# Kernel tuning notes

Measured on AMD Instinct MI355X. Metric: run time of the kernel, lower is better.

The kernel has to match this reference:

```python
import jax, jax.numpy as jnp
import numpy as np

B, S, D = 1, 2048, 4096
H, HKV, HD = 32, 8, 128
MAX_SEQ = 4096
EPS = 1e-5


def rmsnorm(x, w, eps=EPS):
    var = jnp.mean(x * x, axis=-1, keepdims=True)
    return w * (x * jax.lax.rsqrt(var + eps))


def rotate_half_interleaved(x):
    x1 = x[..., ::2]
    x2 = x[..., 1::2]
    return jnp.stack((-x2, x1), axis=-1).reshape(x.shape)


def setup_inputs() -> dict:
    key = jax.random.key(0)
    ks = jax.random.split(key, 8)
    hidden_states = jax.random.normal(ks[0], (B, S, D), dtype=jnp.float32)
    # realistic interleaved RoPE tables: each frequency repeated twice along head_dim
    inv_freq = 1.0 / (10000.0 ** (np.arange(0, HD, 2, dtype=np.float32) / HD))
    pos = np.arange(S, dtype=np.float32)
    ang = pos[:, None] * inv_freq[None, :]            # [S, HD/2]
    ang = np.repeat(ang, 2, axis=-1)                   # [S, HD] interleaved
    cos = jnp.asarray(np.cos(ang))[None].repeat(B, axis=0)  # [B, S, HD]
    sin = jnp.asarray(np.sin(ang))[None].repeat(B, axis=0)
    scale = 1.0 / np.sqrt(D)
    return {
        "hidden_states": hidden_states,
        "cos": cos,
        "sin": sin,
        "k_cache": jnp.zeros((B, MAX_SEQ, HKV, HD), dtype=jnp.float32),
        "v_cache": jnp.zeros((B, MAX_SEQ, HKV, HD), dtype=jnp.float32),
        "Wq": jax.random.normal(ks[1], (D, H * HD), dtype=jnp.float32) * scale,
        "Wk": jax.random.normal(ks[2], (D, HKV * HD), dtype=jnp.float32) * scale,
        "Wv": jax.random.normal(ks[3], (D, HKV * HD), dtype=jnp.float32) * scale,
        "Wo": jax.random.normal(ks[4], (H * HD, D), dtype=jnp.float32) * scale,
        "rms_weight": jnp.ones((D,), dtype=jnp.float32),
        "position_ids": jnp.arange(S, dtype=jnp.int64 if jax.config.jax_enable_x64 else jnp.int32),
        "seq_len": S,
    }


def reference(hidden_states, cos, sin, k_cache, v_cache, Wq, Wk, Wv, Wo,
              rms_weight, position_ids, seq_len):
    residual = hidden_states
    h = rmsnorm(hidden_states, rms_weight)
    b, s = h.shape[:2]

    q = jnp.einsum('bsd,de->bse', h, Wq).reshape(b, s, H, HD)
    k = jnp.einsum('bsd,de->bse', h, Wk).reshape(b, s, HKV, HD)
    v = jnp.einsum('bsd,de->bse', h, Wv).reshape(b, s, HKV, HD)

    # interleaved RoPE, cos/sin broadcast over head axis (unsqueeze_dim=-2)
    c = cos[:, :, None, :]
    si = sin[:, :, None, :]
    q = q * c + rotate_half_interleaved(q) * si
    k = k * c + rotate_half_interleaved(k) * si

    # KV-cache scatter at position_ids (repeat_factor == 1 here)
    k_cache_new = k_cache.at[:, position_ids].set(k)
    v_cache_new = v_cache.at[:, position_ids].set(v)

    # prefill path (new_tok_seq_len > 1): causal SDPA with GQA over fresh K/V
    group = H // HKV
    k_full = jnp.repeat(k, group, axis=2)  # [b, s, H, HD]
    v_full = jnp.repeat(v, group, axis=2)
    qh = q.transpose(0, 2, 1, 3)           # bhqd
    kh = k_full.transpose(0, 2, 1, 3)
    vh = v_full.transpose(0, 2, 1, 3)
    scores = jnp.einsum('bhqd,bhkd->bhqk', qh, kh) / jnp.sqrt(jnp.float32(HD))
    causal = jnp.tril(jnp.ones((s, s), dtype=bool))
    scores = jnp.where(causal[None, None], scores, jnp.finfo(scores.dtype).min)
    probs = jax.nn.softmax(scores, axis=-1)
    attn = jnp.einsum('bhqk,bhkd->bhqd', probs, vh)
    attn = attn.transpose(0, 2, 1, 3).reshape(b, s, H * HD)

    out = jnp.einsum('bse,ed->bsd', attn, Wo)
    with_residual = residual + out
    return with_residual, k_cache_new, v_cache_new
```

## Files before the change

### kernel.cpp

```cpp
#include <hip/hip_runtime.h>
#include <hip/hip_bf16.h>
#include <cstdint>

#define S_LEN 2048
#define DMODEL 4096
#define NHEAD 32
#define NKV 8
#define HDIM 128
#define MAXSEQ 4096
#define NQKV 6144

typedef __bf16 bf16x8 __attribute__((ext_vector_type(8)));
typedef float f32x4 __attribute__((ext_vector_type(4)));
typedef short s16x4 __attribute__((ext_vector_type(4)));

__device__ __forceinline__ short f2bf(float f) {
  unsigned u = __builtin_bit_cast(unsigned, f);
  u += 0x7fffu + ((u >> 16) & 1u);
  return (short)(u >> 16);
}

__device__ __forceinline__ void gload_lds16(const void* g, const void* l) {
  __builtin_amdgcn_global_load_lds((const __attribute__((address_space(1))) unsigned*)g,
                                   (__attribute__((address_space(3))) unsigned*)(l), 16, 0, 0);
}

__global__ __launch_bounds__(256) void rmsnorm_kernel(const float* __restrict__ x,
                                                      const float* __restrict__ w,
                                                      short* __restrict__ out) {
  const int row = blockIdx.x, tid = threadIdx.x;
  const float4* xr = (const float4*)(x + (size_t)row * DMODEL);
  const float4* wr = (const float4*)w;
  float4 v[4];
  float ss = 0.f;
#pragma unroll
  for (int i = 0; i < 4; ++i) {
    v[i] = xr[tid + i * 256];
    ss += v[i].x * v[i].x + v[i].y * v[i].y + v[i].z * v[i].z + v[i].w * v[i].w;
  }
#pragma unroll
  for (int m = 32; m; m >>= 1) ss += __shfl_down(ss, m, 64);
  __shared__ float red[4];
  if ((tid & 63) == 0) red[tid >> 6] = ss;
  __syncthreads();
  float tot = red[0] + red[1] + red[2] + red[3];
  float sc = rsqrtf(tot * (1.f / DMODEL) + 1e-5f);
#pragma unroll
  for (int i = 0; i < 4; ++i) {
    float4 wv = wr[tid + i * 256];
    s16x4 o;
    o[0] = f2bf(v[i].x * sc * wv.x);
    o[1] = f2bf(v[i].y * sc * wv.y);
    o[2] = f2bf(v[i].z * sc * wv.z);
    o[3] = f2bf(v[i].w * sc * wv.w);
    *(s16x4*)&out[(size_t)row * DMODEL + (size_t)(tid + i * 256) * 4] = o;
  }
}

__global__ __launch_bounds__(256) void cast_transpose(const float* __restrict__ src,
                                                      short* __restrict__ dst,
                                                      int rows, int cols) {
  __shared__ float tile[32][33];
  const int c0 = blockIdx.x * 32, r0 = blockIdx.y * 32;
  const int tx = threadIdx.x, ty = threadIdx.y;
#pragma unroll
  for (int i = ty; i < 32; i += 8) tile[i][tx] = src[(size_t)(r0 + i) * cols + c0 + tx];
  __syncthreads();
  const int tid = ty * 32 + tx;
#pragma unroll
  for (int rep = 0; rep < 2; ++rep) {
    int w = rep * 256 + tid;
    int i = w >> 4, pr = (w & 15) * 2;
    short2 o;
    o.x = f2bf(tile[pr][i]);
    o.y = f2bf(tile[pr + 1][i]);
    *(short2*)&dst[(size_t)(c0 + i) * rows + r0 + pr] = o;
  }
}

__global__ __launch_bounds__(256) void v_transpose(const float* __restrict__ QKV,
                                                   float* __restrict__ vc,
                                                   short* __restrict__ vt) {
  __shared__ float tile[32][33];
  const int d0 = blockIdx.x * 32, s0 = blockIdx.y * 32, g = blockIdx.z;
  const int tx = threadIdx.x, ty = threadIdx.y;
#pragma unroll
  for (int i = ty; i < 32; i += 8) {
    float v = QKV[(size_t)(s0 + i) * NQKV + (NHEAD + NKV) * HDIM + g * HDIM + d0 + tx];
    tile[i][tx] = v;
    vc[(size_t)(s0 + i) * (NKV * HDIM) + g * HDIM + d0 + tx] = v;
  }
  __syncthreads();
  const int tid = ty * 32 + tx;
#pragma unroll
  for (int rep = 0; rep < 2; ++rep) {
    int w = rep * 256 + tid;
    int i = w >> 4, pr = (w & 15) * 2;
    short2 o;
    o.x = f2bf(tile[pr][i]);
    o.y = f2bf(tile[pr + 1][i]);
    *(short2*)&vt[((size_t)g * HDIM + d0 + i) * S_LEN + s0 + pr] = o;
  }
}


template<int KS, int MH>
__device__ __forceinline__ void ph_load(const short* __restrict__ AsH, const short* __restrict__ BsH,
                                        const int lrow, const int quad, const int brow0,
                                        bf16x8 (&aR)[4], bf16x8 (&bR)[2][4]) {
  const int xr = lrow & 7;
#pragma unroll
  for (int f = 0; f < 4; ++f)
    aR[f] = *(const bf16x8*)&AsH[((((MH * 4 + f) * 16 + lrow) * 8) + ((KS * 4 + quad) ^ xr)) * 8];
  if constexpr (KS == 0 && MH == 0) {
#pragma unroll
    for (int ks = 0; ks < 2; ++ks)
#pragma unroll
      for (int f = 0; f < 4; ++f)
        bR[ks][f] = *(const bf16x8*)&BsH[(((brow0 + f * 16 + lrow) * 8) + ((ks * 4 + quad) ^ xr)) * 8];
  }
}

template<int KS, int MH>
__device__ __forceinline__ void ph_mfma(bf16x8 (&aR)[4], bf16x8 (&bR)[2][4], f32x4 (&acc)[8][4]) {
#pragma unroll
  for (int f = 0; f < 4; ++f)
#pragma unroll
    for (int n = 0; n < 4; ++n)
      acc[MH * 4 + f][n] =
          __builtin_amdgcn_mfma_f32_16x16x32_bf16(aR[f], bR[KS][n], acc[MH * 4 + f][n], 0, 0, 0);
}

__global__ __launch_bounds__(512, 2) void gemm256(const short* __restrict__ A,
                                                  const short* __restrict__ Bt,
                                                  float* __restrict__ C,
                                                  const float* __restrict__ resid,
                                                  int M, int N, int K) {
  extern __shared__ __align__(16) short smem[];
  short* As = smem;
  short* Bs = smem + 32768;
  const int tid = threadIdx.x;
  const int lane = tid & 63, wave = tid >> 6;
  const int wm = wave >> 2, wn = wave & 3;
  const int lrow = lane & 15, quad = lane >> 4;
  const int bhalf = wn >> 1, brow0 = (wn & 1) * 64;
  const int m0 = blockIdx.y * 256, n0 = blockIdx.x * 256;
  const int srow = tid >> 3;
  const int scol = ((tid & 7) ^ (srow & 7)) << 3;
  const short* Ag = A + (size_t)m0 * K;
  const short* Bg = Bt + (size_t)n0 * K;
  const int nk = K >> 6;

#define STAGE_A(b, h, kt) do { \
    const short* g_ = Ag + (size_t)((h) * 128 + srow) * K + (size_t)(kt) * 64 + scol; \
    short* l_ = As + ((b) * 2 + (h)) * 8192 + wave * 512; \
    gload_lds16(g_, l_); \
    gload_lds16(g_ + (size_t)64 * K, l_ + 4096); \
  } while (0)
#define STAGE_B(b, h, kt) do { \
    const short* g_ = Bg + (size_t)((h) * 128 + srow) * K + (size_t)(kt) * 64 + scol; \
    short* l_ = Bs + ((b) * 2 + (h)) * 8192 + wave * 512; \
    gload_lds16(g_, l_); \
    gload_lds16(g_ + (size_t)64 * K, l_ + 4096); \
  } while (0)
#define VW_NONE
#define VW_4 asm volatile("s_waitcnt vmcnt(4)" ::: "memory");
#define VW_COND if (more) { asm volatile("s_waitcnt vmcnt(4)" ::: "memory"); } \
                else      { asm volatile("s_waitcnt vmcnt(0)" ::: "memory"); }
#define PHASE(BUF, KS, MH, STMT, VW) \
  ph_load<KS, MH>(As + ((BUF) * 2 + wm) * 8192, Bs + ((BUF) * 2 + bhalf) * 8192, \
                  lrow, quad, brow0, aR, bR); \
  STMT; \
  VW \
  __builtin_amdgcn_s_barrier(); \
  asm volatile("s_waitcnt lgkmcnt(0)" ::: "memory"); \
  __builtin_amdgcn_s_setprio(1); \
  ph_mfma<KS, MH>(aR, bR, acc); \
  __builtin_amdgcn_s_setprio(0); \
  __builtin_amdgcn_s_barrier();

  f32x4 acc[8][4] = {};
  bf16x8 aR[4], bR[2][4];

  STAGE_A(0, 0, 0); STAGE_A(0, 1, 0);
  STAGE_B(0, 0, 0); STAGE_B(0, 1, 0);
  STAGE_B(1, 0, 1); STAGE_B(1, 1, 1);
  asm volatile("s_waitcnt vmcnt(4)" ::: "memory");
  __builtin_amdgcn_s_barrier();

  const int niter = nk >> 1;
  for (int i = 0; i < niter; ++i) {
    const int t = 2 * i;
    const bool more = (t + 2 < nk);
    PHASE(0, 0, 0, STAGE_A(1, 0, t + 1), VW_NONE)
    PHASE(0, 0, 1, STAGE_A(1, 1, t + 1), VW_NONE)
    PHASE(0, 1, 0, if (more) { STAGE_B(0, 0, t + 2); }, VW_NONE)
    PHASE(0, 1, 1, if (more) { STAGE_B(0, 1, t + 2); }, VW_COND)
    PHASE(1, 0, 0, if (more) { STAGE_A(0, 0, t + 2); }, VW_NONE)
    PHASE(1, 0, 1, if (more) { STAGE_A(0, 1, t + 2); }, VW_NONE)
    PHASE(1, 1, 0, if (more) { STAGE_B(1, 0, t + 3); }, VW_NONE)
    PHASE(1, 1, 1, if (more) { STAGE_B(1, 1, t + 3); }, VW_4)
  }

#pragma unroll
  for (int fm = 0; fm < 8; ++fm)
#pragma unroll
    for (int fn = 0; fn < 4; ++fn) {
      int row = m0 + wm * 128 + fm * 16 + quad * 4;
      int col = n0 + wn * 64 + fn * 16 + lrow;
#pragma unroll
      for (int r = 0; r < 4; ++r) {
        float v = acc[fm][fn][r];
        size_t o = (size_t)(row + r) * N + col;
        if (resid) v += resid[o];
        C[o] = v;
      }
    }
#undef STAGE_A
#undef STAGE_B
#undef VW_NONE
#undef VW_4
#undef VW_COND
#undef PHASE
}

__global__ __launch_bounds__(256) void rope_kernel(const float* __restrict__ QKV,
                                                   const float* __restrict__ cosb,
                                                   const float* __restrict__ sinb,
                                                   short* __restrict__ qo,
                                                   short* __restrict__ ko,
                                                   float* __restrict__ kc,
                                                   float* __restrict__ vc) {
  const int s = blockIdx.x, tid = threadIdx.x;
  const float4* r4 = (const float4*)(QKV + (size_t)s * NQKV);
  const float qscale = 0.08838834764831845f;
#pragma unroll
  for (int it = 0; it < 5; ++it) {
    int i = it * 256 + tid;
    float4 x = r4[i];
    int e = i * 4;
    int d = e & 127;
    float4 c = *(const float4*)&cosb[(size_t)s * HDIM + d];
    float4 si = *(const float4*)&sinb[(size_t)s * HDIM + d];
    float o0 = x.x * c.x - x.y * si.x;
    float o1 = x.y * c.y + x.x * si.y;
    float o2 = x.z * c.z - x.w * si.z;
    float o3 = x.w * c.w + x.z * si.w;
    if (e < NHEAD * HDIM) {
      int hh = e >> 7;
      s16x4 ov;
      ov[0] = f2bf(o0 * qscale); ov[1] = f2bf(o1 * qscale);
      ov[2] = f2bf(o2 * qscale); ov[3] = f2bf(o3 * qscale);
      *(s16x4*)&qo[((size_t)hh * S_LEN + s) * HDIM + d] = ov;
    } else {
      int ek = e - NHEAD * HDIM;
      int g = ek >> 7;
      s16x4 ov;
      ov[0] = f2bf(o0); ov[1] = f2bf(o1); ov[2] = f2bf(o2); ov[3] = f2bf(o3);
      *(s16x4*)&ko[((size_t)g * S_LEN + s) * HDIM + d] = ov;
      *(float4*)&kc[(size_t)s * (NKV * HDIM) + ek] = make_float4(o0, o1, o2, o3);
    }
  }
  {
    const size_t base = (size_t)S_LEN * NKV * HDIM;
    const size_t i = (size_t)s * 256 + tid;
    const float4 z = make_float4(0.f, 0.f, 0.f, 0.f);
    ((float4*)(kc + base))[i] = z;
    ((float4*)(vc + base))[i] = z;
  }
}

#define TKEY 128
__global__ __launch_bounds__(256, 1) void attn_kernel(const short* __restrict__ Q,
                                                      const short* __restrict__ Kb,
                                                      const short* __restrict__ Vt,
                                                      short* __restrict__ out) {
  extern __shared__ __align__(16) short smem[];
  short* Ks = smem;
  short* Vs = smem + 32768;
  short* Ps = smem + 65536;
  const int tid = threadIdx.x;
  const int lane = tid & 63, wave = tid >> 6;
  const int lrow = lane & 15, quad = lane >> 4;
  const int g = blockIdx.x & 7, p = blockIdx.x >> 3;
  const int h = g * 4 + wave;
  const float L2E = 1.44269504f;
  const short* Kg = Kb + (size_t)g * S_LEN * HDIM;
  const short* Vg = Vt + (size_t)g * HDIM * S_LEN;
  short* Pw = Ps + wave * 1024;

#pragma unroll 1
  for (int ph = 0; ph < 2; ++ph) {
    const int qt = ph ? (63 - p) : p;
    const int nt = (qt >> 2) + 1;

    bf16x8 qf[2][4];
#pragma unroll
    for (int i = 0; i < 2; ++i)
#pragma unroll
      for (int kf = 0; kf < 4; ++kf)
        qf[i][kf] = *(const bf16x8*)&Q[((size_t)h * S_LEN + qt * 32 + i * 16 + lrow) * HDIM + kf * 32 + quad * 8];

    f32x4 O[2][8] = {};
    float mrun[2][4], lrun[2][4];
#pragma unroll
    for (int i = 0; i < 2; ++i)
#pragma unroll
      for (int r = 0; r < 4; ++r) { mrun[i][r] = -1e30f; lrun[i][r] = 0.f; }

#pragma unroll
    for (int ii = 0; ii < 8; ++ii) {
      int s = (wave * 8 + ii) * 64 + lane;
      int r = s >> 4, gg = (s & 15) ^ (r & 15);
      gload_lds16(Kg + (size_t)r * HDIM + gg * 8, Ks + (wave * 8 + ii) * 512);
    }
#pragma unroll
    for (int ii = 0; ii < 8; ++ii) {
      int s = (wave * 8 + ii) * 64 + lane;
      int d = s >> 4, kg = (s & 15) ^ (d & 15);
      gload_lds16(Vg + (size_t)d * S_LEN + kg * 8, Vs + (wave * 8 + ii) * 512);
    }
    __syncthreads();

#pragma unroll 1
    for (int t = 0; t < nt; ++t) {
      const int bsel = t & 1;
      if (t + 1 < nt) {
        const int kb2 = (t + 1) * TKEY, o = (1 - bsel) * 16384;
#pragma unroll
        for (int ii = 0; ii < 8; ++ii) {
          int s = (wave * 8 + ii) * 64 + lane;
          int r = s >> 4, gg = (s & 15) ^ (r & 15);
          gload_lds16(Kg + (size_t)(kb2 + r) * HDIM + gg * 8, Ks + o + (wave * 8 + ii) * 512);
        }
#pragma unroll
        for (int ii = 0; ii < 8; ++ii) {
          int s = (wave * 8 + ii) * 64 + lane;
          int d = s >> 4, kg = (s & 15) ^ (d & 15);
          gload_lds16(Vg + (size_t)d * S_LEN + kb2 + kg * 8, Vs + o + (wave * 8 + ii) * 512);
        }
      }
      const short* Kc = Ks + bsel * 16384;
      const short* Vc = Vs + bsel * 16384;

      f32x4 sc[2][8] = {};
#pragma unroll
      for (int c = 0; c < 8; ++c) {
        int r = c * 16 + lrow;
#pragma unroll
        for (int kf = 0; kf < 4; ++kf) {
          int slot = r * 16 + ((kf * 4 + quad) ^ lrow);
          bf16x8 kfr = *(const bf16x8*)&Kc[slot * 8];
          sc[0][c] = __builtin_amdgcn_mfma_f32_16x16x32_bf16(qf[0][kf], kfr, sc[0][c], 0, 0, 0);
          sc[1][c] = __builtin_amdgcn_mfma_f32_16x16x32_bf16(qf[1][kf], kfr, sc[1][c], 0, 0, 0);
        }
      }

      const int kb = t * TKEY;
      const bool last = (t == nt - 1);
#pragma unroll
      for (int i = 0; i < 2; ++i) {
        if (last) {
#pragma unroll
          for (int c = 0; c < 8; ++c) {
            int key = kb + c * 16 + lrow;
#pragma unroll
            for (int r = 0; r < 4; ++r) {
              int row = qt * 32 + i * 16 + quad * 4 + r;
              if (key > row) sc[i][c][r] = -1e30f;
            }
          }
        }
        float tm[4];
#pragma unroll
        for (int r = 0; r < 4; ++r) tm[r] = sc[i][0][r];
#pragma unroll
        for (int c = 1; c < 8; ++c)
#pragma unroll
          for (int r = 0; r < 4; ++r) tm[r] = fmaxf(tm[r], sc[i][c][r]);
#pragma unroll
        for (int msk = 1; msk <= 8; msk <<= 1)
#pragma unroll
          for (int r = 0; r < 4; ++r) tm[r] = fmaxf(tm[r], __shfl_xor(tm[r], msk, 64));
#pragma unroll
        for (int r = 0; r < 4; ++r) {
          float nm = fmaxf(mrun[i][r], tm[r]);
          float alpha = exp2f((mrun[i][r] - nm) * L2E);
          mrun[i][r] = nm;
          lrun[i][r] *= alpha;
#pragma unroll
          for (int jd = 0; jd < 8; ++jd) O[i][jd][r] *= alpha;
        }
        float rs[4] = {0.f, 0.f, 0.f, 0.f};
#pragma unroll
        for (int c = 0; c < 8; ++c)
#pragma unroll
          for (int r = 0; r < 4; ++r) {
            float pv = exp2f((sc[i][c][r] - mrun[i][r]) * L2E);
            sc[i][c][r] = pv;
            rs[r] += pv;
          }
#pragma unroll
        for (int msk = 1; msk <= 8; msk <<= 1)
#pragma unroll
          for (int r = 0; r < 4; ++r) rs[r] += __shfl_xor(rs[r], msk, 64);
#pragma unroll
        for (int r = 0; r < 4; ++r) lrun[i][r] += rs[r];
      }

#pragma unroll
      for (int ks = 0; ks < 4; ++ks) {
#pragma unroll
        for (int i = 0; i < 2; ++i)
#pragma unroll
          for (int cc = 0; cc < 2; ++cc) {
            int c = ks * 2 + cc;
            int kg = cc * 2 + (lrow >> 3), off = lrow & 7;
#pragma unroll
            for (int r = 0; r < 4; ++r) {
              int q2 = i * 16 + quad * 4 + r;
              int slot = q2 * 4 + (kg ^ (q2 & 3) ^ ((q2 >> 2) & 3));
              Pw[slot * 8 + off] = f2bf(sc[i][c][r]);
            }
          }
        bf16x8 pa[2];
#pragma unroll
        for (int i = 0; i < 2; ++i) {
          int q2 = i * 16 + lrow;
          int slot = q2 * 4 + (quad ^ (q2 & 3) ^ ((q2 >> 2) & 3));
          pa[i] = *(const bf16x8*)&Pw[slot * 8];
        }
#pragma unroll
        for (int jd = 0; jd < 8; ++jd) {
          int d = jd * 16 + lrow;
          int slotv = d * 16 + ((ks * 4 + quad) ^ lrow);
          bf16x8 vb = *(const bf16x8*)&Vc[slotv * 8];
          O[0][jd] = __builtin_amdgcn_mfma_f32_16x16x32_bf16(pa[0], vb, O[0][jd], 0, 0, 0);
          O[1][jd] = __builtin_amdgcn_mfma_f32_16x16x32_bf16(pa[1], vb, O[1][jd], 0, 0, 0);
        }
      }
      __syncthreads();
    }

#pragma unroll
    for (int i = 0; i < 2; ++i)
#pragma unroll
      for (int r = 0; r < 4; ++r) {
        float inv = 1.f / lrun[i][r];
        int row = qt * 32 + i * 16 + quad * 4 + r;
#pragma unroll
        for (int jd = 0; jd < 8; ++jd)
          out[(size_t)row * DMODEL + h * HDIM + jd * 16 + lrow] = f2bf(O[i][jd][r] * inv);
      }
    __syncthreads();
  }
}

extern "C" void kernel_launch(void* const* d_in, const int* in_sizes, int n_in,
                              void* d_out, int out_size, void* d_ws, size_t ws_size,
                              hipStream_t stream) {
  const float* hs   = (const float*)d_in[0];
  const float* cosb = (const float*)d_in[1];
  const float* sinb = (const float*)d_in[2];
  const float* Wq   = (const float*)d_in[5];
  const float* Wk   = (const float*)d_in[6];
  const float* Wv   = (const float*)d_in[7];
  const float* Wo   = (const float*)d_in[8];
  const float* rmsw = (const float*)d_in[9];

  float* outp = (float*)d_out;
  float* kc = outp + (size_t)S_LEN * DMODEL;
  float* vc = kc + (size_t)MAXSEQ * NKV * HDIM;

  char* p = (char*)d_ws;
  short* h_bf  = (short*)p; p += (size_t)S_LEN * DMODEL * 2;
  short* WqkvT = (short*)p; p += (size_t)NQKV * DMODEL * 2;
  short* WoT   = (short*)p; p += (size_t)DMODEL * DMODEL * 2;
  float* QKV   = (float*)p; p += (size_t)S_LEN * NQKV * 4;
  short* q_bf  = (short*)p; p += (size_t)NHEAD * S_LEN * HDIM * 2;
  short* k_bf  = (short*)p; p += (size_t)NKV * S_LEN * HDIM * 2;
  short* vt_bf = (short*)p; p += (size_t)NKV * HDIM * S_LEN * 2;
  short* attn_bf = h_bf;

  const int ATTN_LDS = 139264;
  hipFuncSetAttribute(reinterpret_cast<const void*>(attn_kernel),
                      hipFuncAttributeMaxDynamicSharedMemorySize, ATTN_LDS);
  const int GEMM_LDS = 131072;
  hipFuncSetAttribute(reinterpret_cast<const void*>(gemm256),
                      hipFuncAttributeMaxDynamicSharedMemorySize, GEMM_LDS);

  rmsnorm_kernel<<<S_LEN, 256, 0, stream>>>(hs, rmsw, h_bf);
  cast_transpose<<<dim3(DMODEL / 32, DMODEL / 32), dim3(32, 8), 0, stream>>>(Wq, WqkvT, DMODEL, DMODEL);
  cast_transpose<<<dim3(1024 / 32, DMODEL / 32), dim3(32, 8), 0, stream>>>(Wk, WqkvT + (size_t)DMODEL * DMODEL, DMODEL, 1024);
  cast_transpose<<<dim3(1024 / 32, DMODEL / 32), dim3(32, 8), 0, stream>>>(Wv, WqkvT + (size_t)5120 * DMODEL, DMODEL, 1024);
  cast_transpose<<<dim3(DMODEL / 32, DMODEL / 32), dim3(32, 8), 0, stream>>>(Wo, WoT, DMODEL, DMODEL);
  gemm256<<<dim3(NQKV / 256, S_LEN / 256), 512, GEMM_LDS, stream>>>(h_bf, WqkvT, QKV, nullptr, S_LEN, NQKV, DMODEL);
  rope_kernel<<<S_LEN, 256, 0, stream>>>(QKV, cosb, sinb, q_bf, k_bf, kc, vc);
  v_transpose<<<dim3(HDIM / 32, S_LEN / 32, NKV), dim3(32, 8), 0, stream>>>(QKV, vc, vt_bf);
  attn_kernel<<<256, 256, ATTN_LDS, stream>>>(q_bf, k_bf, vt_bf, attn_bf);
  gemm256<<<dim3(DMODEL / 256, S_LEN / 256), 512, GEMM_LDS, stream>>>(attn_bf, WoT, outp, hs, S_LEN, DMODEL, DMODEL);
}
```

Before: 675.3 us.

## Templatize GEMM N-tile width and merge weight cast-transpose launches

The 256x256 GEMM gets a template parameter for N fragments per wave, so the QKV projection uses 256x192 tiles (256 blocks) and the output projection uses 256x128 tiles (256 blocks). The aim is to fill all CUs, where 256-wide N tiles left too few blocks (192 and 128). B-tile staging, the LDS layout and the vmcnt waits are reworked for a variable number of 64-row B groups. The four weight cast-transpose launches become one 3D-grid launch with early exit for out-of-range blocks. Narrower N tiles lower arithmetic intensity per block and add A-tile reloads.

```diff
diff --git a/kernel.cpp b/kernel.cpp
--- a/kernel.cpp
+++ b/kernel.cpp
@@ -23,6 +23,14 @@
 __device__ __forceinline__ void gload_lds16(const void* g, const void* l) {
   __builtin_amdgcn_global_load_lds((const __attribute__((address_space(1))) unsigned*)g,
                                    (__attribute__((address_space(3))) unsigned*)(l), 16, 0, 0);
+}
+
+template<int N> __device__ __forceinline__ void vwait() {
+  if constexpr (N == 0) asm volatile("s_waitcnt vmcnt(0)" ::: "memory");
+  else if constexpr (N == 1) asm volatile("s_waitcnt vmcnt(1)" ::: "memory");
+  else if constexpr (N == 2) asm volatile("s_waitcnt vmcnt(2)" ::: "memory");
+  else if constexpr (N == 3) asm volatile("s_waitcnt vmcnt(3)" ::: "memory");
+  else if constexpr (N == 4) asm volatile("s_waitcnt vmcnt(4)" ::: "memory");
 }
 
 __global__ __launch_bounds__(256) void rmsnorm_kernel(const float* __restrict__ x,
@@ -57,11 +65,23 @@
   }
 }
 
-__global__ __launch_bounds__(256) void cast_transpose(const float* __restrict__ src,
-                                                      short* __restrict__ dst,
-                                                      int rows, int cols) {
+__global__ __launch_bounds__(256) void cast_transpose_all(const float* __restrict__ Wq,
+                                                          const float* __restrict__ Wk,
+                                                          const float* __restrict__ Wv,
+                                                          const float* __restrict__ Wo,
+                                                          short* __restrict__ WqkvT,
+                                                          short* __restrict__ WoT) {
+  const int z = blockIdx.z;
+  const float* src;
+  short* dst;
+  int cols;
+  if (z == 0)      { src = Wq; dst = WqkvT;                            cols = 4096; }
+  else if (z == 1) { src = Wk; dst = WqkvT + (size_t)4096 * 4096;      cols = 1024; }
+  else if (z == 2) { src = Wv; dst = WqkvT + (size_t)5120 * 4096;      cols = 1024; }
+  else             { src = Wo; dst = WoT;                              cols = 4096; }
+  const int c0 = blockIdx.x * 32, r0 = blockIdx.y * 32;
+  if (c0 >= cols) return;
   __shared__ float tile[32][33];
-  const int c0 = blockIdx.x * 32, r0 = blockIdx.y * 32;
   const int tx = threadIdx.x, ty = threadIdx.y;
 #pragma unroll
   for (int i = ty; i < 32; i += 8) tile[i][tx] = src[(size_t)(r0 + i) * cols + c0 + tx];
@@ -74,7 +94,7 @@
     short2 o;
     o.x = f2bf(tile[pr][i]);
     o.y = f2bf(tile[pr + 1][i]);
-    *(short2*)&dst[(size_t)(c0 + i) * rows + r0 + pr] = o;
+    *(short2*)&dst[(size_t)(c0 + i) * 4096 + r0 + pr] = o;
   }
 }
 
@@ -104,33 +124,34 @@
 }
 
 
-template<int KS, int MH>
-__device__ __forceinline__ void ph_load(const short* __restrict__ AsH, const short* __restrict__ BsH,
-                                        const int lrow, const int quad, const int brow0,
-                                        bf16x8 (&aR)[4], bf16x8 (&bR)[2][4]) {
+template<int NF, int KS, int MH>
+__device__ __forceinline__ void ph_load(const short* __restrict__ AsH, const short* __restrict__ BsB,
+                                        const int lrow, const int quad, const int wn,
+                                        bf16x8 (&aR)[4], bf16x8 (&bR)[2][NF]) {
   const int xr = lrow & 7;
 #pragma unroll
   for (int f = 0; f < 4; ++f)
     aR[f] = *(const bf16x8*)&AsH[((((MH * 4 + f) * 16 + lrow) * 8) + ((KS * 4 + quad) ^ xr)) * 8];
-  if constexpr (KS == 0 && MH == 0) {
-#pragma unroll
-    for (int ks = 0; ks < 2; ++ks)
-#pragma unroll
-      for (int f = 0; f < 4; ++f)
-        bR[ks][f] = *(const bf16x8*)&BsH[(((brow0 + f * 16 + lrow) * 8) + ((ks * 4 + quad) ^ xr)) * 8];
-  }
-}
-
-template<int KS, int MH>
-__device__ __forceinline__ void ph_mfma(bf16x8 (&aR)[4], bf16x8 (&bR)[2][4], f32x4 (&acc)[8][4]) {
+  if constexpr (MH == 0) {
+#pragma unroll
+    for (int f = 0; f < NF; ++f) {
+      int rB = wn * (16 * NF) + f * 16 + lrow;
+      bR[KS][f] = *(const bf16x8*)&BsB[((rB * 8) + ((KS * 4 + quad) ^ xr)) * 8];
+    }
+  }
+}
+
+template<int NF, int KS, int MH>
+__device__ __forceinline__ void ph_mfma(bf16x8 (&aR)[4], bf16x8 (&bR)[2][NF], f32x4 (&acc)[8][NF]) {
 #pragma unroll
   for (int f = 0; f < 4; ++f)
 #pragma unroll
-    for (int n = 0; n < 4; ++n)
+    for (int n = 0; n < NF; ++n)
       acc[MH * 4 + f][n] =
           __builtin_amdgcn_mfma_f32_16x16x32_bf16(aR[f], bR[KS][n], acc[MH * 4 + f][n], 0, 0, 0);
 }
 
+template<int NF>
 __global__ __launch_bounds__(512, 2) void gemm256(const short* __restrict__ A,
                                                   const short* __restrict__ Bt,
                                                   float* __restrict__ C,
@@ -143,13 +164,14 @@
   const int lane = tid & 63, wave = tid >> 6;
   const int wm = wave >> 2, wn = wave & 3;
   const int lrow = lane & 15, quad = lane >> 4;
-  const int bhalf = wn >> 1, brow0 = (wn & 1) * 64;
-  const int m0 = blockIdx.y * 256, n0 = blockIdx.x * 256;
+  const int m0 = blockIdx.y * 256, n0 = blockIdx.x * (64 * NF);
   const int srow = tid >> 3;
   const int scol = ((tid & 7) ^ (srow & 7)) << 3;
   const short* Ag = A + (size_t)m0 * K;
   const short* Bg = Bt + (size_t)n0 * K;
   const int nk = K >> 6;
+  constexpr int G1 = NF - (NF >> 1);
+  constexpr int G2 = NF >> 1;
 
 #define STAGE_A(b, h, kt) do { \
     const short* g_ = Ag + (size_t)((h) * 128 + srow) * K + (size_t)(kt) * 64 + scol; \
@@ -157,57 +179,61 @@
     gload_lds16(g_, l_); \
     gload_lds16(g_ + (size_t)64 * K, l_ + 4096); \
   } while (0)
-#define STAGE_B(b, h, kt) do { \
-    const short* g_ = Bg + (size_t)((h) * 128 + srow) * K + (size_t)(kt) * 64 + scol; \
-    short* l_ = Bs + ((b) * 2 + (h)) * 8192 + wave * 512; \
+#define STAGE_BG(b, gr, kt) do { \
+    const short* g_ = Bg + (size_t)((gr) * 64 + srow) * K + (size_t)(kt) * 64 + scol; \
+    short* l_ = Bs + (b) * (NF * 4096) + (gr) * 4096 + wave * 512; \
     gload_lds16(g_, l_); \
-    gload_lds16(g_ + (size_t)64 * K, l_ + 4096); \
   } while (0)
-#define VW_NONE
-#define VW_4 asm volatile("s_waitcnt vmcnt(4)" ::: "memory");
-#define VW_COND if (more) { asm volatile("s_waitcnt vmcnt(4)" ::: "memory"); } \
-                else      { asm volatile("s_waitcnt vmcnt(0)" ::: "memory"); }
+#define VW_COND if (more) { vwait<NF>(); } else { vwait<0>(); }
 #define PHASE(BUF, KS, MH, STMT, VW) \
-  ph_load<KS, MH>(As + ((BUF) * 2 + wm) * 8192, Bs + ((BUF) * 2 + bhalf) * 8192, \
-                  lrow, quad, brow0, aR, bR); \
+  ph_load<NF, KS, MH>(As + ((BUF) * 2 + wm) * 8192, Bs + (BUF) * (NF * 4096), \
+                      lrow, quad, wn, aR, bR); \
   STMT; \
   VW \
   __builtin_amdgcn_s_barrier(); \
   asm volatile("s_waitcnt lgkmcnt(0)" ::: "memory"); \
   __builtin_amdgcn_s_setprio(1); \
-  ph_mfma<KS, MH>(aR, bR, acc); \
+  ph_mfma<NF, KS, MH>(aR, bR, acc); \
   __builtin_amdgcn_s_setprio(0); \
   __builtin_amdgcn_s_barrier();
 
-  f32x4 acc[8][4] = {};
-  bf16x8 aR[4], bR[2][4];
+  f32x4 acc[8][NF] = {};
+  bf16x8 aR[4], bR[2][NF];
 
   STAGE_A(0, 0, 0); STAGE_A(0, 1, 0);
-  STAGE_B(0, 0, 0); STAGE_B(0, 1, 0);
-  STAGE_B(1, 0, 1); STAGE_B(1, 1, 1);
-  asm volatile("s_waitcnt vmcnt(4)" ::: "memory");
+#pragma unroll
+  for (int g = 0; g < NF; ++g) STAGE_BG(0, g, 0);
+#pragma unroll
+  for (int g = 0; g < NF; ++g) STAGE_BG(1, g, 1);
+  vwait<NF>();
   __builtin_amdgcn_s_barrier();
 
   const int niter = nk >> 1;
   for (int i = 0; i < niter; ++i) {
     const int t = 2 * i;
     const bool more = (t + 2 < nk);
-    PHASE(0, 0, 0, STAGE_A(1, 0, t + 1), VW_NONE)
-    PHASE(0, 0, 1, STAGE_A(1, 1, t + 1), VW_NONE)
-    PHASE(0, 1, 0, if (more) { STAGE_B(0, 0, t + 2); }, VW_NONE)
-    PHASE(0, 1, 1, if (more) { STAGE_B(0, 1, t + 2); }, VW_COND)
-    PHASE(1, 0, 0, if (more) { STAGE_A(0, 0, t + 2); }, VW_NONE)
-    PHASE(1, 0, 1, if (more) { STAGE_A(0, 1, t + 2); }, VW_NONE)
-    PHASE(1, 1, 0, if (more) { STAGE_B(1, 0, t + 3); }, VW_NONE)
-    PHASE(1, 1, 1, if (more) { STAGE_B(1, 1, t + 3); }, VW_4)
+    PHASE(0, 0, 0, STAGE_A(1, 0, t + 1), )
+    PHASE(0, 0, 1, STAGE_A(1, 1, t + 1), )
+    PHASE(0, 1, 0,
+          if (more) { _Pragma("unroll") for (int g = 0; g < G1; ++g) STAGE_BG(0, g, t + 2); }, )
+    PHASE(0, 1, 1,
+          if (more) { _Pragma("unroll") for (int g = G1; g < NF; ++g) STAGE_BG(0, g, t + 2); },
+          VW_COND)
+    PHASE(1, 0, 0, if (more) { STAGE_A(0, 0, t + 2); }, )
+    PHASE(1, 0, 1, if (more) { STAGE_A(0, 1, t + 2); }, )
+    PHASE(1, 1, 0,
+          if (more) { _Pragma("unroll") for (int g = 0; g < G1; ++g) STAGE_BG(1, g, t + 3); }, )
+    PHASE(1, 1, 1,
+          if (more) { _Pragma("unroll") for (int g = G1; g < NF; ++g) STAGE_BG(1, g, t + 3); },
+          vwait<NF>();)
   }
 
 #pragma unroll
   for (int fm = 0; fm < 8; ++fm)
 #pragma unroll
-    for (int fn = 0; fn < 4; ++fn) {
+    for (int fn = 0; fn < NF; ++fn) {
       int row = m0 + wm * 128 + fm * 16 + quad * 4;
-      int col = n0 + wn * 64 + fn * 16 + lrow;
+      int col = n0 + wn * (16 * NF) + fn * 16 + lrow;
 #pragma unroll
       for (int r = 0; r < 4; ++r) {
         float v = acc[fm][fn][r];
@@ -217,9 +243,7 @@
       }
     }
 #undef STAGE_A
-#undef STAGE_B
-#undef VW_NONE
-#undef VW_4
+#undef STAGE_BG
 #undef VW_COND
 #undef PHASE
 }
@@ -485,18 +509,18 @@
   const int ATTN_LDS = 139264;
   hipFuncSetAttribute(reinterpret_cast<const void*>(attn_kernel),
                       hipFuncAttributeMaxDynamicSharedMemorySize, ATTN_LDS);
-  const int GEMM_LDS = 131072;
-  hipFuncSetAttribute(reinterpret_cast<const void*>(gemm256),
-                      hipFuncAttributeMaxDynamicSharedMemorySize, GEMM_LDS);
+  const int GEMM_LDS3 = 65536 + 3 * 16384;
+  const int GEMM_LDS2 = 65536 + 2 * 16384;
+  hipFuncSetAttribute(reinterpret_cast<const void*>(gemm256<3>),
+                      hipFuncAttributeMaxDynamicSharedMemorySize, GEMM_LDS3);
+  hipFuncSetAttribute(reinterpret_cast<const void*>(gemm256<2>),
+                      hipFuncAttributeMaxDynamicSharedMemorySize, GEMM_LDS2);
 
   rmsnorm_kernel<<<S_LEN, 256, 0, stream>>>(hs, rmsw, h_bf);
-  cast_transpose<<<dim3(DMODEL / 32, DMODEL / 32), dim3(32, 8), 0, stream>>>(Wq, WqkvT, DMODEL, DMODEL);
-  cast_transpose<<<dim3(1024 / 32, DMODEL / 32), dim3(32, 8), 0, stream>>>(Wk, WqkvT + (size_t)DMODEL * DMODEL, DMODEL, 1024);
-  cast_transpose<<<dim3(1024 / 32, DMODEL / 32), dim3(32, 8), 0, stream>>>(Wv, WqkvT + (size_t)5120 * DMODEL, DMODEL, 1024);
-  cast_transpose<<<dim3(DMODEL / 32, DMODEL / 32), dim3(32, 8), 0, stream>>>(Wo, WoT, DMODEL, DMODEL);
-  gemm256<<<dim3(NQKV / 256, S_LEN / 256), 512, GEMM_LDS, stream>>>(h_bf, WqkvT, QKV, nullptr, S_LEN, NQKV, DMODEL);
+  cast_transpose_all<<<dim3(128, 128, 4), dim3(32, 8), 0, stream>>>(Wq, Wk, Wv, Wo, WqkvT, WoT);
+  gemm256<3><<<dim3(NQKV / 192, S_LEN / 256), 512, GEMM_LDS3, stream>>>(h_bf, WqkvT, QKV, nullptr, S_LEN, NQKV, DMODEL);
   rope_kernel<<<S_LEN, 256, 0, stream>>>(QKV, cosb, sinb, q_bf, k_bf, kc, vc);
   v_transpose<<<dim3(HDIM / 32, S_LEN / 32, NKV), dim3(32, 8), 0, stream>>>(QKV, vc, vt_bf);
   attn_kernel<<<256, 256, ATTN_LDS, stream>>>(q_bf, k_bf, vt_bf, attn_bf);
-  gemm256<<<dim3(DMODEL / 256, S_LEN / 256), 512, GEMM_LDS, stream>>>(attn_bf, WoT, outp, hs, S_LEN, DMODEL, DMODEL);
-}
+  gemm256<2><<<dim3(DMODEL / 128, S_LEN / 256), 512, GEMM_LDS2, stream>>>(attn_bf, WoT, outp, hs, S_LEN, DMODEL, DMODEL);
+}
```

Result: faster. 586.7 us (-13.1%).
